# Performance work log

Hardware: AMD Instinct MI355X
Metric: run time of the kernel (lower is better)

Reference implementation:

```python
import jax, jax.numpy as jnp
import numpy as np

N = 50000      # nodes
E = 800000     # edges
IN = 256       # in_channels
OUT = 128      # out_channels
HID = 2 * OUT  # hidden = 2*out_channels


def setup_inputs() -> dict:
    key = jax.random.key(0)
    ks = jax.random.split(key, 8)
    x = jax.random.normal(ks[0], (N, IN), dtype=jnp.float32)
    edge_index = jax.random.randint(ks[1], (2, E), 0, N, dtype=jnp.int32)
    def glorot(k, fan_in, fan_out):
        return jax.random.normal(k, (fan_in, fan_out), jnp.float32) * np.float32(1.0 / np.sqrt(fan_in))
    W1 = glorot(ks[2], IN, HID)
    b1 = jnp.zeros((HID,), jnp.float32)
    Wmu = glorot(ks[3], HID, OUT)
    bmu = jnp.zeros((OUT,), jnp.float32)
    Wls = glorot(ks[4], HID, OUT)
    bls = jnp.zeros((OUT,), jnp.float32)
    return {"x": x, "edge_index": edge_index, "W1": W1, "b1": b1,
            "Wmu": Wmu, "bmu": bmu, "Wls": Wls, "bls": bls}


def reference(x, edge_index, W1, b1, Wmu, bmu, Wls, bls):
    n = x.shape[0]
    # add self-loops (PyG GCNConv default add_self_loops=True)
    loop = jnp.arange(n, dtype=edge_index.dtype)
    src = jnp.concatenate([edge_index[0], loop])  # message sources (row)
    dst = jnp.concatenate([edge_index[1], loop])  # aggregation targets (col)
    # symmetric normalization: deg over targets, norm = d^-1/2[src] * d^-1/2[dst]
    deg = jax.ops.segment_sum(jnp.ones(src.shape[0], x.dtype), dst, num_segments=n)
    dinv = jnp.where(deg > 0, jax.lax.rsqrt(deg), 0.0)
    norm = dinv[src] * dinv[dst]  # [E+N]

    def gcn(h, W, b):
        h = h @ W                                   # [N, F_out] dense transform
        msg = h[src] * norm[:, None]                # gather + scale   [E+N, F_out]
        agg = jax.ops.segment_sum(msg, dst, num_segments=n)  # scatter-add
        return agg + b

    h = jax.nn.relu(gcn(x, W1, b1))
    return gcn(h, Wmu, bmu), gcn(h, Wls, bls)
```

## Files before the change

### kernel.cpp

```cpp
#include <hip/hip_runtime.h>
#include <hip/hip_fp16.h>

typedef __attribute__((ext_vector_type(8))) _Float16 half8;
typedef __attribute__((ext_vector_type(4))) float float4v;

#define LDP 40


__global__ __launch_bounds__(256) void k_deg(const int* __restrict__ dst, int* __restrict__ deg, int E) {
    int e = blockIdx.x * 256 + threadIdx.x;
    if (e < E) atomicAdd(&deg[dst[e]], 1);
}


__global__ __launch_bounds__(256) void k_scan1(const int* __restrict__ deg, int* __restrict__ rowptr,
                                               int* __restrict__ bsum, float* __restrict__ dinv, int N) {
    __shared__ int sm[256];
    const int t = threadIdx.x;
    const int i = blockIdx.x * 256 + t;
    int v = (i < N) ? deg[i] : 0;
    if (i < N) dinv[i] = rsqrtf((float)(v + 1));
    int x = v;
    sm[t] = x;
    __syncthreads();
#pragma unroll
    for (int off = 1; off < 256; off <<= 1) {
        int y = (t >= off) ? sm[t - off] : 0;
        __syncthreads();
        x += y;
        sm[t] = x;
        __syncthreads();
    }
    if (i < N) rowptr[i] = x - v;
    if (t == 255) bsum[blockIdx.x] = x;
}

__global__ __launch_bounds__(256) void k_scan2(int* __restrict__ bsum, int* __restrict__ rowptr, int nb, int N) {
    __shared__ int sm[256];
    const int t = threadIdx.x;
    int v = (t < nb) ? bsum[t] : 0;
    int x = v;
    sm[t] = x;
    __syncthreads();
#pragma unroll
    for (int off = 1; off < 256; off <<= 1) {
        int y = (t >= off) ? sm[t - off] : 0;
        __syncthreads();
        x += y;
        sm[t] = x;
        __syncthreads();
    }
    if (t < nb) bsum[t] = x - v;
    if (t == 255) rowptr[N] = x;
}

__global__ __launch_bounds__(256) void k_scan3(int* __restrict__ rowptr, const int* __restrict__ bsum, int N) {
    int i = blockIdx.x * 256 + threadIdx.x;
    if (i < N) rowptr[i] += bsum[blockIdx.x];
}

__global__ __launch_bounds__(256) void k_fill(const int* __restrict__ src, const int* __restrict__ dst,
                                              const int* __restrict__ rowptr, int* __restrict__ rowcnt,
                                              int* __restrict__ csr, int E) {
    int e = blockIdx.x * 256 + threadIdx.x;
    if (e < E) {
        int d = dst[e];
        int pos = rowptr[d] + atomicAdd(&rowcnt[d], 1);
        csr[pos] = src[e];
    }
}

__global__ __launch_bounds__(256) void k_wt(const float* __restrict__ W1, const float* __restrict__ Wmu,
                                            const float* __restrict__ Wls, _Float16* __restrict__ Wt1,
                                            _Float16* __restrict__ Wct) {
    int b = blockIdx.x;
    int t = threadIdx.x;
    if (b < 256) {
        Wt1[b * 256 + t] = (_Float16)W1[t * 256 + b];
    } else {
        int j = b - 256;
        float v = (j < 128) ? Wmu[t * 128 + j] : Wls[t * 128 + (j - 128)];
        Wct[j * 256 + t] = (_Float16)v;
    }
}

template <int AF32, int OUTF32>
__global__ __launch_bounds__(256) void gemm_k(const void* __restrict__ Aptr, const _Float16* __restrict__ Bt,
                                              const float* __restrict__ bmu, const float* __restrict__ bls,
                                              void* __restrict__ outp, int M, size_t split) {
    __shared__ _Float16 As[128 * LDP];
    __shared__ _Float16 Bs[128 * LDP];
    const int t = threadIdx.x;
    const int lane = t & 63;
    const int wid = t >> 6;
    const int bm = blockIdx.x * 128;
    const int bn = blockIdx.y * 128;
    const int wm = (wid & 1) * 64;
    const int wn = (wid >> 1) * 64;

    float4v acc[4][4];
#pragma unroll
    for (int i = 0; i < 4; i++)
#pragma unroll
        for (int j = 0; j < 4; j++) acc[i][j] = (float4v){0.f, 0.f, 0.f, 0.f};

    for (int kt = 0; kt < 256; kt += 32) {
        if (AF32) {
            const float* A = (const float*)Aptr;
            int row = t >> 1;
            int ko = (t & 1) * 16;
            int gr = bm + row; if (gr >= M) gr = M - 1;
            const float4v* p = (const float4v*)(A + (size_t)gr * 256 + kt + ko);
            float4v v0 = p[0], v1 = p[1], v2 = p[2], v3 = p[3];
            half8 h0, h1;
            h0[0] = (_Float16)v0[0]; h0[1] = (_Float16)v0[1]; h0[2] = (_Float16)v0[2]; h0[3] = (_Float16)v0[3];
            h0[4] = (_Float16)v1[0]; h0[5] = (_Float16)v1[1]; h0[6] = (_Float16)v1[2]; h0[7] = (_Float16)v1[3];
            h1[0] = (_Float16)v2[0]; h1[1] = (_Float16)v2[1]; h1[2] = (_Float16)v2[2]; h1[3] = (_Float16)v2[3];
            h1[4] = (_Float16)v3[0]; h1[5] = (_Float16)v3[1]; h1[6] = (_Float16)v3[2]; h1[7] = (_Float16)v3[3];
            *(half8*)&As[row * LDP + ko] = h0;
            *(half8*)&As[row * LDP + ko + 8] = h1;
        } else {
            const _Float16* A = (const _Float16*)Aptr;
#pragma unroll
            for (int m = 0; m < 2; m++) {
                int c = t + m * 256;
                int row = c >> 2, ks = (c & 3) * 8;
                int gr = bm + row; if (gr >= M) gr = M - 1;
                half8 v = *(const half8*)(A + (size_t)gr * 256 + kt + ks);
                *(half8*)&As[row * LDP + ks] = v;
            }
        }
#pragma unroll
        for (int m = 0; m < 2; m++) {
            int c = t + m * 256;
            int row = c >> 2, ks = (c & 3) * 8;
            half8 v = *(const half8*)(Bt + (size_t)(bn + row) * 256 + kt + ks);
            *(half8*)&Bs[row * LDP + ks] = v;
        }
        __syncthreads();

        const int kg = (lane >> 4) * 8;
        const int fr = lane & 15;
        half8 af[4], bf[4];
#pragma unroll
        for (int f = 0; f < 4; f++) af[f] = *(const half8*)&As[(wm + f * 16 + fr) * LDP + kg];
#pragma unroll
        for (int f = 0; f < 4; f++) bf[f] = *(const half8*)&Bs[(wn + f * 16 + fr) * LDP + kg];
#pragma unroll
        for (int i = 0; i < 4; i++)
#pragma unroll
            for (int j = 0; j < 4; j++)
                acc[i][j] = __builtin_amdgcn_mfma_f32_16x16x32_f16(af[i], bf[j], acc[i][j], 0, 0, 0);
        __syncthreads();
    }

    const int fc = lane & 15;
    const int rq = (lane >> 4) * 4;
    if (OUTF32) {
        float* out = (float*)outp;
#pragma unroll
        for (int i = 0; i < 4; i++) {
#pragma unroll
            for (int j = 0; j < 4; j++) {
                int col = bn + wn + j * 16 + fc;
                float bias = (col < 128) ? bmu[col] : bls[col - 128];
#pragma unroll
                for (int r = 0; r < 4; r++) {
                    int row = bm + wm + i * 16 + rq + r;
                    if (row < M) {
                        size_t o = (col < 128) ? ((size_t)row * 128 + col)
                                               : (split + (size_t)row * 128 + (col - 128));
                        out[o] = acc[i][j][r] + bias;
                    }
                }
            }
        }
    } else {
        _Float16* out = (_Float16*)outp;
#pragma unroll
        for (int i = 0; i < 4; i++) {
#pragma unroll
            for (int j = 0; j < 4; j++) {
                int col = bn + wn + j * 16 + fc;
#pragma unroll
                for (int r = 0; r < 4; r++) {
                    int row = bm + wm + i * 16 + rq + r;
                    if (row < M) out[(size_t)row * 256 + col] = (_Float16)acc[i][j][r];
                }
            }
        }
    }
}

__global__ __launch_bounds__(256) void k_agg(const _Float16* __restrict__ in, _Float16* __restrict__ out,
                                             const float* __restrict__ dinv, const int* __restrict__ rowptr,
                                             const int* __restrict__ csr, const float* __restrict__ bias,
                                             int relu, int N) {
    int g = blockIdx.x * 8 + (threadIdx.x >> 5);
    int lane = threadIdx.x & 31;
    if (g >= N) return;
    float dd = dinv[g];
    int beg = rowptr[g], end = rowptr[g + 1];

    float acc[8];
    {
        half8 hv = *(const half8*)(in + (size_t)g * 256 + lane * 8);
        float ws = dd * dd;
#pragma unroll
        for (int j = 0; j < 8; j++) acc[j] = (float)hv[j] * ws;
    }
    for (int e = beg; e < end; ++e) {
        int s = csr[e];
        float w = dinv[s] * dd;
        half8 v = *(const half8*)(in + (size_t)s * 256 + lane * 8);
#pragma unroll
        for (int j = 0; j < 8; j++) acc[j] += (float)v[j] * w;
    }
    if (bias) {
#pragma unroll
        for (int j = 0; j < 8; j++) acc[j] += bias[lane * 8 + j];
    }
    if (relu) {
#pragma unroll
        for (int j = 0; j < 8; j++) acc[j] = fmaxf(acc[j], 0.f);
    }
    half8 o;
#pragma unroll
    for (int j = 0; j < 8; j++) o[j] = (_Float16)acc[j];
    *(half8*)(out + (size_t)g * 256 + lane * 8) = o;
}


extern "C" void kernel_launch(void* const* d_in, const int* in_sizes, int n_in,
                              void* d_out, int out_size, void* d_ws, size_t ws_size,
                              hipStream_t stream) {
    const float* x   = (const float*)d_in[0];
    const int*   ei  = (const int*)d_in[1];
    const float* W1  = (const float*)d_in[2];
    const float* b1  = (const float*)d_in[3];
    const float* Wmu = (const float*)d_in[4];
    const float* bmu = (const float*)d_in[5];
    const float* Wls = (const float*)d_in[6];
    const float* bls = (const float*)d_in[7];
    const int N = in_sizes[0] / 256;
    const int E = in_sizes[1] / 2;
    const int* esrc = ei;
    const int* edst = ei + E;

    char* ws = (char*)d_ws;
    size_t off = 0;
    auto alloc = [&](size_t bytes) -> void* {
        void* p = ws + off;
        off += (bytes + 255) & ~(size_t)255;
        return p;
    };
    _Float16* h1  = (_Float16*)alloc((size_t)N * 256 * 2);
    _Float16* hb  = (_Float16*)alloc((size_t)N * 256 * 2);
    _Float16* Wt1 = (_Float16*)alloc(256 * 256 * 2);
    _Float16* Wct = (_Float16*)alloc(256 * 256 * 2);
    float* dinv   = (float*)alloc((size_t)N * 4);
    int* degcnt   = (int*)alloc((size_t)N * 2 * 4);
    int* deg      = degcnt;
    int* rowcnt   = degcnt + N;
    int* rowptr   = (int*)alloc((size_t)(N + 1) * 4);
    int* bsum     = (int*)alloc(256 * 4);
    int* csr      = (int*)alloc((size_t)E * 4);

    const int nb = (N + 255) / 256;

    hipMemsetAsync(degcnt, 0, (size_t)N * 2 * 4, stream);

    k_deg<<<(E + 255) / 256, 256, 0, stream>>>(edst, deg, E);
    k_scan1<<<nb, 256, 0, stream>>>(deg, rowptr, bsum, dinv, N);
    k_scan2<<<1, 256, 0, stream>>>(bsum, rowptr, nb, N);
    k_scan3<<<nb, 256, 0, stream>>>(rowptr, bsum, N);
    k_fill<<<(E + 255) / 256, 256, 0, stream>>>(esrc, edst, rowptr, rowcnt, csr, E);
    k_wt<<<512, 256, 0, stream>>>(W1, Wmu, Wls, Wt1, Wct);

    dim3 gg((N + 127) / 128, 2);
    gemm_k<1, 0><<<gg, 256, 0, stream>>>(x, Wt1, nullptr, nullptr, h1, N, 0);
    k_agg<<<(N + 7) / 8, 256, 0, stream>>>(h1, hb, dinv, rowptr, csr, b1, 1, N);
    k_agg<<<(N + 7) / 8, 256, 0, stream>>>(hb, h1, dinv, rowptr, csr, nullptr, 0, N);
    gemm_k<0, 1><<<gg, 256, 0, stream>>>(h1, Wct, bmu, bls, d_out, N, (size_t)N * 128);
}
```

Before: 373.0 us.

## Prescale GCN features by dinv, drop per-edge weights, prefetch GEMM tiles

The symmetric normalization is refactored so rows are pre-multiplied by dinv in the GEMM epilogue and in the first aggregation's output. The aggregation then only sums neighbor rows and scales once by the destination dinv, which removes the per-edge dinv gather and multiply. The aggregation also uses a 64-lane wave per node with half4 loads and a 4-way unrolled edge loop. The GEMM moves to a 64-wide K tile with register prefetch of the next tile, overlapping global loads with MFMA at the cost of more registers and LDS.

```diff
diff --git a/kernel.cpp b/kernel.cpp
--- a/kernel.cpp
+++ b/kernel.cpp
@@ -2,9 +2,10 @@
 #include <hip/hip_fp16.h>
 
 typedef __attribute__((ext_vector_type(8))) _Float16 half8;
+typedef __attribute__((ext_vector_type(4))) _Float16 half4;
 typedef __attribute__((ext_vector_type(4))) float float4v;
 
-#define LDP 40
+#define LDP2 72
 
 
 __global__ __launch_bounds__(256) void k_deg(const int* __restrict__ dst, int* __restrict__ deg, int E) {
@@ -87,9 +88,10 @@
 template <int AF32, int OUTF32>
 __global__ __launch_bounds__(256) void gemm_k(const void* __restrict__ Aptr, const _Float16* __restrict__ Bt,
                                               const float* __restrict__ bmu, const float* __restrict__ bls,
+                                              const float* __restrict__ dinv,
                                               void* __restrict__ outp, int M, size_t split) {
-    __shared__ _Float16 As[128 * LDP];
-    __shared__ _Float16 Bs[128 * LDP];
+    __shared__ _Float16 As[128 * LDP2];
+    __shared__ _Float16 Bs[128 * LDP2];
     const int t = threadIdx.x;
     const int lane = t & 63;
     const int wid = t >> 6;
@@ -104,54 +106,86 @@
 #pragma unroll
         for (int j = 0; j < 4; j++) acc[i][j] = (float4v){0.f, 0.f, 0.f, 0.f};
 
-    for (int kt = 0; kt < 256; kt += 32) {
+    float4v ar32[8];
+    half8 ar16[4];
+    half8 br[4];
+
+    const int a32row = t >> 1;
+    const int a32ko = (t & 1) * 32;
+
+    auto load_regs = [&](int kt) {
         if (AF32) {
             const float* A = (const float*)Aptr;
-            int row = t >> 1;
-            int ko = (t & 1) * 16;
-            int gr = bm + row; if (gr >= M) gr = M - 1;
-            const float4v* p = (const float4v*)(A + (size_t)gr * 256 + kt + ko);
-            float4v v0 = p[0], v1 = p[1], v2 = p[2], v3 = p[3];
-            half8 h0, h1;
-            h0[0] = (_Float16)v0[0]; h0[1] = (_Float16)v0[1]; h0[2] = (_Float16)v0[2]; h0[3] = (_Float16)v0[3];
-            h0[4] = (_Float16)v1[0]; h0[5] = (_Float16)v1[1]; h0[6] = (_Float16)v1[2]; h0[7] = (_Float16)v1[3];
-            h1[0] = (_Float16)v2[0]; h1[1] = (_Float16)v2[1]; h1[2] = (_Float16)v2[2]; h1[3] = (_Float16)v2[3];
-            h1[4] = (_Float16)v3[0]; h1[5] = (_Float16)v3[1]; h1[6] = (_Float16)v3[2]; h1[7] = (_Float16)v3[3];
-            *(half8*)&As[row * LDP + ko] = h0;
-            *(half8*)&As[row * LDP + ko + 8] = h1;
+            int gr = bm + a32row; if (gr >= M) gr = M - 1;
+            const float4v* p = (const float4v*)(A + (size_t)gr * 256 + kt + a32ko);
+#pragma unroll
+            for (int q = 0; q < 8; q++) ar32[q] = p[q];
         } else {
             const _Float16* A = (const _Float16*)Aptr;
 #pragma unroll
-            for (int m = 0; m < 2; m++) {
-                int c = t + m * 256;
-                int row = c >> 2, ks = (c & 3) * 8;
+            for (int m = 0; m < 4; m++) {
+                int u = m * 256 + t;
+                int row = u >> 3, k8 = (u & 7) * 8;
                 int gr = bm + row; if (gr >= M) gr = M - 1;
-                half8 v = *(const half8*)(A + (size_t)gr * 256 + kt + ks);
-                *(half8*)&As[row * LDP + ks] = v;
-            }
-        }
-#pragma unroll
-        for (int m = 0; m < 2; m++) {
-            int c = t + m * 256;
-            int row = c >> 2, ks = (c & 3) * 8;
-            half8 v = *(const half8*)(Bt + (size_t)(bn + row) * 256 + kt + ks);
-            *(half8*)&Bs[row * LDP + ks] = v;
-        }
-        __syncthreads();
+                ar16[m] = *(const half8*)(A + (size_t)gr * 256 + kt + k8);
+            }
+        }
+#pragma unroll
+        for (int m = 0; m < 4; m++) {
+            int u = m * 256 + t;
+            int row = u >> 3, k8 = (u & 7) * 8;
+            br[m] = *(const half8*)(Bt + (size_t)(bn + row) * 256 + kt + k8);
+        }
+    };
+
+    auto write_lds = [&]() {
+        if (AF32) {
+#pragma unroll
+            for (int q = 0; q < 4; q++) {
+                half8 h;
+#pragma unroll
+                for (int j = 0; j < 4; j++) { h[j] = (_Float16)ar32[2 * q][j]; h[4 + j] = (_Float16)ar32[2 * q + 1][j]; }
+                *(half8*)&As[a32row * LDP2 + a32ko + q * 8] = h;
+            }
+        } else {
+#pragma unroll
+            for (int m = 0; m < 4; m++) {
+                int u = m * 256 + t;
+                int row = u >> 3, k8 = (u & 7) * 8;
+                *(half8*)&As[row * LDP2 + k8] = ar16[m];
+            }
+        }
+#pragma unroll
+        for (int m = 0; m < 4; m++) {
+            int u = m * 256 + t;
+            int row = u >> 3, k8 = (u & 7) * 8;
+            *(half8*)&Bs[row * LDP2 + k8] = br[m];
+        }
+    };
+
+    load_regs(0);
+#pragma unroll
+    for (int it = 0; it < 4; it++) {
+        if (it > 0) __syncthreads();
+        write_lds();
+        __syncthreads();
+        if (it < 3) load_regs((it + 1) * 64);
 
         const int kg = (lane >> 4) * 8;
         const int fr = lane & 15;
-        half8 af[4], bf[4];
-#pragma unroll
-        for (int f = 0; f < 4; f++) af[f] = *(const half8*)&As[(wm + f * 16 + fr) * LDP + kg];
-#pragma unroll
-        for (int f = 0; f < 4; f++) bf[f] = *(const half8*)&Bs[(wn + f * 16 + fr) * LDP + kg];
-#pragma unroll
-        for (int i = 0; i < 4; i++)
-#pragma unroll
-            for (int j = 0; j < 4; j++)
-                acc[i][j] = __builtin_amdgcn_mfma_f32_16x16x32_f16(af[i], bf[j], acc[i][j], 0, 0, 0);
-        __syncthreads();
+#pragma unroll
+        for (int kk = 0; kk < 64; kk += 32) {
+            half8 af[4], bf[4];
+#pragma unroll
+            for (int f = 0; f < 4; f++) af[f] = *(const half8*)&As[(wm + f * 16 + fr) * LDP2 + kk + kg];
+#pragma unroll
+            for (int f = 0; f < 4; f++) bf[f] = *(const half8*)&Bs[(wn + f * 16 + fr) * LDP2 + kk + kg];
+#pragma unroll
+            for (int i = 0; i < 4; i++)
+#pragma unroll
+                for (int j = 0; j < 4; j++)
+                    acc[i][j] = __builtin_amdgcn_mfma_f32_16x16x32_f16(af[i], bf[j], acc[i][j], 0, 0, 0);
+        }
     }
 
     const int fc = lane & 15;
@@ -180,12 +214,15 @@
 #pragma unroll
         for (int i = 0; i < 4; i++) {
 #pragma unroll
-            for (int j = 0; j < 4; j++) {
-                int col = bn + wn + j * 16 + fc;
-#pragma unroll
-                for (int r = 0; r < 4; r++) {
-                    int row = bm + wm + i * 16 + rq + r;
-                    if (row < M) out[(size_t)row * 256 + col] = (_Float16)acc[i][j][r];
+            for (int r = 0; r < 4; r++) {
+                int row = bm + wm + i * 16 + rq + r;
+                if (row < M) {
+                    float sc = dinv[row];
+#pragma unroll
+                    for (int j = 0; j < 4; j++) {
+                        int col = bn + wn + j * 16 + fc;
+                        out[(size_t)row * 256 + col] = (_Float16)(acc[i][j][r] * sc);
+                    }
                 }
             }
         }
@@ -195,39 +232,50 @@
 __global__ __launch_bounds__(256) void k_agg(const _Float16* __restrict__ in, _Float16* __restrict__ out,
                                              const float* __restrict__ dinv, const int* __restrict__ rowptr,
                                              const int* __restrict__ csr, const float* __restrict__ bias,
-                                             int relu, int N) {
-    int g = blockIdx.x * 8 + (threadIdx.x >> 5);
-    int lane = threadIdx.x & 31;
+                                             int mode, int N) {
+    const int g = blockIdx.x * 4 + (threadIdx.x >> 6);
+    const int lane = threadIdx.x & 63;
     if (g >= N) return;
-    float dd = dinv[g];
-    int beg = rowptr[g], end = rowptr[g + 1];
-
-    float acc[8];
+    const float dd = dinv[g];
+    const int beg = rowptr[g], end = rowptr[g + 1];
+    const size_t fo = (size_t)lane * 4;
+
+    float acc[4];
     {
-        half8 hv = *(const half8*)(in + (size_t)g * 256 + lane * 8);
-        float ws = dd * dd;
-#pragma unroll
-        for (int j = 0; j < 8; j++) acc[j] = (float)hv[j] * ws;
-    }
-    for (int e = beg; e < end; ++e) {
+        half4 hv = *(const half4*)(in + (size_t)g * 256 + fo);
+#pragma unroll
+        for (int j = 0; j < 4; j++) acc[j] = (float)hv[j];
+    }
+    int e = beg;
+    for (; e + 4 <= end; e += 4) {
+        int s0 = csr[e], s1 = csr[e + 1], s2 = csr[e + 2], s3 = csr[e + 3];
+        half4 v0 = *(const half4*)(in + (size_t)s0 * 256 + fo);
+        half4 v1 = *(const half4*)(in + (size_t)s1 * 256 + fo);
+        half4 v2 = *(const half4*)(in + (size_t)s2 * 256 + fo);
+        half4 v3 = *(const half4*)(in + (size_t)s3 * 256 + fo);
+#pragma unroll
+        for (int j = 0; j < 4; j++)
+            acc[j] += (float)v0[j] + (float)v1[j] + (float)v2[j] + (float)v3[j];
+    }
+    for (; e < end; ++e) {
         int s = csr[e];
-        float w = dinv[s] * dd;
-        half8 v = *(const half8*)(in + (size_t)s * 256 + lane * 8);
-#pragma unroll
-        for (int j = 0; j < 8; j++) acc[j] += (float)v[j] * w;
-    }
-    if (bias) {
-#pragma unroll
-        for (int j = 0; j < 8; j++) acc[j] += bias[lane * 8 + j];
-    }
-    if (relu) {
-#pragma unroll
-        for (int j = 0; j < 8; j++) acc[j] = fmaxf(acc[j], 0.f);
-    }
-    half8 o;
-#pragma unroll
-    for (int j = 0; j < 8; j++) o[j] = (_Float16)acc[j];
-    *(half8*)(out + (size_t)g * 256 + lane * 8) = o;
+        half4 v = *(const half4*)(in + (size_t)s * 256 + fo);
+#pragma unroll
+        for (int j = 0; j < 4; j++) acc[j] += (float)v[j];
+    }
+
+    half4 o;
+    if (mode) {
+#pragma unroll
+        for (int j = 0; j < 4; j++) {
+            float r = fmaxf(acc[j] * dd + bias[lane * 4 + j], 0.f);
+            o[j] = (_Float16)(r * dd);
+        }
+    } else {
+#pragma unroll
+        for (int j = 0; j < 4; j++) o[j] = (_Float16)(acc[j] * dd);
+    }
+    *(half4*)(out + (size_t)g * 256 + fo) = o;
 }
 
 
@@ -278,8 +326,8 @@
     k_wt<<<512, 256, 0, stream>>>(W1, Wmu, Wls, Wt1, Wct);
 
     dim3 gg((N + 127) / 128, 2);
-    gemm_k<1, 0><<<gg, 256, 0, stream>>>(x, Wt1, nullptr, nullptr, h1, N, 0);
-    k_agg<<<(N + 7) / 8, 256, 0, stream>>>(h1, hb, dinv, rowptr, csr, b1, 1, N);
-    k_agg<<<(N + 7) / 8, 256, 0, stream>>>(hb, h1, dinv, rowptr, csr, nullptr, 0, N);
-    gemm_k<0, 1><<<gg, 256, 0, stream>>>(h1, Wct, bmu, bls, d_out, N, (size_t)N * 128);
-}
+    gemm_k<1, 0><<<gg, 256, 0, stream>>>(x, Wt1, nullptr, nullptr, dinv, h1, N, 0);
+    k_agg<<<(N + 3) / 4, 256, 0, stream>>>(h1, hb, dinv, rowptr, csr, b1, 1, N);
+    k_agg<<<(N + 3) / 4, 256, 0, stream>>>(hb, h1, dinv, rowptr, csr, nullptr, 0, N);
+    gemm_k<0, 1><<<gg, 256, 0, stream>>>(h1, Wct, bmu, bls, nullptr, d_out, N, (size_t)N * 128);
+}
```

After: 360.7 us. 1.03x faster.
